# Kernel optimization log

Measured on AMD Instinct MI355X. Metric: run time of the kernel, lower is better.

Reference implementation:

```python
import jax, jax.numpy as jnp
import numpy as np

B, L, H = 2, 2048, 2048
NH, NKV, HD = 16, 8, 128
K = 4            # conv kernel size
BASE = 1000000.0 # rotary base
H2 = NH // 2
N_REP = NH // NKV


def setup_inputs() -> dict:
    key = jax.random.key(0)
    ks = jax.random.split(key, 12)
    s = 0.02
    hidden_states = jax.random.normal(ks[0], (B, L, H), jnp.float32)
    idx = jnp.arange(L)
    diff = (idx[:, None] - idx[None, :]).astype(jnp.float32)
    # lightning-attention decay mask: -(i-j) on/below diagonal, -1e9 above
    lin_attention_mask = jnp.where(diff >= 0, -diff, -1e9).astype(jnp.float32)
    # additive causal mask for softmax half
    attention_mask = jnp.where(diff >= 0, 0.0, -1e9).astype(jnp.float32)[None, None]
    # ALiBi-style positive per-head slopes for the linear half
    slope_rate = (2.0 ** (-8.0 * jnp.arange(1, H2 + 1, dtype=jnp.float32) / H2)).reshape(H2, 1, 1)
    position_ids = jnp.arange(L, dtype=jnp.int32)
    Wq = s * jax.random.normal(ks[1], (H, H), jnp.float32)
    bq = jnp.zeros((H,), jnp.float32)
    Wk = s * jax.random.normal(ks[2], (H, NKV * HD), jnp.float32)
    bk = jnp.zeros((NKV * HD,), jnp.float32)
    Wv = s * jax.random.normal(ks[3], (H, NKV * HD), jnp.float32)
    bv = jnp.zeros((NKV * HD,), jnp.float32)
    Wo = s * jax.random.normal(ks[4], (H, H), jnp.float32)
    # conv init: identity tap at last index + tiny noise (matches _init_conv_to_one)
    q_conv_w = jnp.zeros((H // 2, K), jnp.float32).at[:, K - 1].set(1.0) + 1e-4 * jax.random.normal(ks[5], (H // 2, K), jnp.float32)
    q_conv_b = jnp.zeros((H // 2,), jnp.float32)
    k_conv_w = jnp.zeros((NKV * HD, K), jnp.float32).at[:, K - 1].set(1.0) + 1e-4 * jax.random.normal(ks[6], (NKV * HD, K), jnp.float32)
    k_conv_b = jnp.zeros((NKV * HD,), jnp.float32)
    return dict(hidden_states=hidden_states, lin_attention_mask=lin_attention_mask,
                attention_mask=attention_mask, slope_rate=slope_rate, position_ids=position_ids,
                Wq=Wq, bq=bq, Wk=Wk, bk=bk, Wv=Wv, bv=bv, Wo=Wo,
                q_conv_w=q_conv_w, q_conv_b=q_conv_b, k_conv_w=k_conv_w, k_conv_b=k_conv_b)


def _dwconv_causal(x, w, b):
    # x: [B,L,C]; w: [C,K]; b: [C]. Causal depthwise conv (torch Conv1d cross-correlation,
    # padding K-1 then truncate to first L positions).
    xp = jnp.pad(x, ((0, 0), (K - 1, 0), (0, 0)))
    y = b
    for i in range(K):
        y = y + xp[:, i:i + x.shape[1], :] * w[:, i]
    return y


def _rot_half(x):
    return jnp.concatenate([-x[..., HD // 2:], x[..., :HD // 2]], axis=-1)


def _rep_kv(x):
    # [B,NKV,L,D] -> [B,NH,L,D] via repeat_interleave on head dim
    return jnp.repeat(x, N_REP, axis=1)


def reference(hidden_states, lin_attention_mask, attention_mask, slope_rate, position_ids,
              Wq, bq, Wk, bk, Wv, bv, Wo, q_conv_w, q_conv_b, k_conv_w, k_conv_b):
    q = hidden_states @ Wq + bq          # [B,L,H]
    k = hidden_states @ Wk + bk          # [B,L,NKV*HD]
    v = hidden_states @ Wv + bv          # [B,L,NKV*HD]

    # ---- softmax half (first NH//2 heads, rotary) ----
    qs = q[..., :H // 2].reshape(B, L, H2, HD).transpose(0, 2, 1, 3)   # [B,H2,L,D]
    ks_ = k.reshape(B, L, NKV, HD).transpose(0, 2, 1, 3)               # [B,NKV,L,D]
    vs = v.reshape(B, L, NKV, HD).transpose(0, 2, 1, 3)
    inv_freq = 1.0 / (BASE ** (jnp.arange(0, HD, 2, dtype=jnp.float32) / HD))
    freqs = position_ids.astype(jnp.float32)[:, None] * inv_freq[None, :]
    emb = jnp.concatenate([freqs, freqs], axis=-1)                     # [L,D]
    cos, sin = jnp.cos(emb)[None, None], jnp.sin(emb)[None, None]
    qs = qs * cos + _rot_half(qs) * sin
    kr = ks_ * cos + _rot_half(ks_) * sin
    k_soft = _rep_kv(kr)[:, :H2]
    v_soft = _rep_kv(vs)[:, :H2]
    attn = jnp.einsum('bhnd,bhmd->bhnm', qs, k_soft) / np.sqrt(HD).astype(np.float32)
    attn = attn + attention_mask
    attn = jax.nn.softmax(attn.astype(jnp.float32), axis=-1).astype(qs.dtype)
    attn_out = jnp.einsum('bhnm,bhmd->bhnd', attn, v_soft)
    attn_out = attn_out.transpose(0, 2, 1, 3).reshape(B, L, H // 2)

    # ---- linear half (last NH//2 heads: conv -> silu -> decayed linear attention) ----
    q_tnorm = _dwconv_causal(q[..., H // 2:], q_conv_w, q_conv_b)      # [B,L,H/2]
    kc = _dwconv_causal(k, k_conv_w, k_conv_b)                          # [B,L,NKV*HD]
    qt = jax.nn.silu(q_tnorm).reshape(B, L, H2, HD).transpose(0, 2, 1, 3)
    kc = jax.nn.silu(kc).reshape(B, L, NKV, HD).transpose(0, 2, 1, 3)
    k_lin = _rep_kv(kc)[:, H2:]
    v_lin = _rep_kv(vs)[:, H2:]
    lin_mask = jnp.exp(slope_rate * lin_attention_mask)                 # [H2,L,L]
    energy = jnp.einsum('bhnd,bhmd->bhnm', qt, k_lin) * lin_mask
    out_t = jnp.einsum('bhnm,bhmd->bhnd', energy, v_lin)
    out_t = out_t.transpose(0, 2, 1, 3).reshape(B, L, H // 2)
    # SimpleRMSNorm (no weight), computed in fp32
    ot32 = out_t.astype(jnp.float32)
    out_t = (ot32 * jax.lax.rsqrt(jnp.mean(ot32 * ot32, axis=-1, keepdims=True) + 1e-6)).astype(out_t.dtype)

    return jnp.concatenate([attn_out, out_t], axis=-1) @ Wo
```

## Files before the change

kernel.cpp:

```cpp
#include <hip/hip_runtime.h>
#include <hip/hip_bf16.h>

typedef __attribute__((ext_vector_type(8))) short short8;
typedef __attribute__((ext_vector_type(4))) float f32x4;
typedef __attribute__((ext_vector_type(16))) float f32x16;

__device__ __forceinline__ void gl_lds16(const void* g, void* l) {
    void* gp = const_cast<void*>(g);
    __builtin_amdgcn_global_load_lds((__attribute__((address_space(1))) void*)gp,
                                     (__attribute__((address_space(3))) void*)l, 16, 0, 0);
}
__device__ __forceinline__ short f2bf(float f) {
    __hip_bfloat16 h = __float2bfloat16(f);
    return __builtin_bit_cast(short, h);
}
__device__ __forceinline__ float bf2f(__hip_bfloat16 h) { return __bfloat162float(h); }
__device__ __forceinline__ float bfbits2f(short s) {
    unsigned int u = ((unsigned int)(unsigned short)s) << 16;
    return __builtin_bit_cast(float, u);
}
__device__ __forceinline__ void store_val(float* C, size_t i, float v) { C[i] = v; }
__device__ __forceinline__ void store_val(__hip_bfloat16* C, size_t i, float v) { C[i] = __float2bfloat16(v); }

__global__ __launch_bounds__(256) void pre_kernel(
    const float* __restrict__ hs, __hip_bfloat16* __restrict__ hsb,
    const float* __restrict__ bq, const float* __restrict__ bk, const float* __restrict__ bv,
    float* __restrict__ bqkv,
    const float* __restrict__ Wq, const float* __restrict__ Wo,
    const float* __restrict__ Wk, const float* __restrict__ Wv,
    __hip_bfloat16* __restrict__ oq, __hip_bfloat16* __restrict__ oo, __hip_bfloat16* __restrict__ okv)
{
    __shared__ float tile[64][65];
    int bx = blockIdx.x, t = threadIdx.x;
    if (bx < 8192) {
        size_t i = (size_t)bx * 256 + t;
        float4 v = ((const float4*)hs)[i];
        ushort4 o;
        o.x = (unsigned short)f2bf(v.x); o.y = (unsigned short)f2bf(v.y);
        o.z = (unsigned short)f2bf(v.z); o.w = (unsigned short)f2bf(v.w);
        ((ushort4*)hsb)[i] = o;
    } else if (bx < 8208) {
        int i = (bx - 8192) * 256 + t;
        bqkv[i] = (i < 2048) ? bq[i] : ((i < 3072) ? bk[i - 2048] : bv[i - 3072]);
    } else {
        int idx = bx - 8208;
        int z = idx >> 10, rem = idx & 1023;
        const float* in; __hip_bfloat16* out; int C;
        if (z == 0)      { in = Wq; out = oq; C = 2048; }
        else if (z == 1) { in = Wo; out = oo; C = 2048; }
        else if (z == 2) { in = Wk; out = okv; C = 1024; }
        else             { in = Wv; out = okv + (size_t)1024 * 2048; C = 1024; }
        int c0 = (rem & 31) * 64, r0 = (rem >> 5) * 64;
        if (c0 >= C) return;
        int tx = t & 15, ty = t >> 4;
#pragma unroll
        for (int i = 0; i < 4; ++i) {
            float4 v = *(const float4*)(in + (size_t)(r0 + ty + i * 16) * C + c0 + tx * 4);
            tile[ty + i * 16][tx * 4 + 0] = v.x; tile[ty + i * 16][tx * 4 + 1] = v.y;
            tile[ty + i * 16][tx * 4 + 2] = v.z; tile[ty + i * 16][tx * 4 + 3] = v.w;
        }
        __syncthreads();
#pragma unroll
        for (int i = 0; i < 4; ++i) {
            int lc = ty + i * 16, lr0 = tx * 4;
            ushort4 o;
            o.x = (unsigned short)f2bf(tile[lr0 + 0][lc]);
            o.y = (unsigned short)f2bf(tile[lr0 + 1][lc]);
            o.z = (unsigned short)f2bf(tile[lr0 + 2][lc]);
            o.w = (unsigned short)f2bf(tile[lr0 + 3][lc]);
            *(ushort4*)(out + (size_t)(c0 + lc) * 2048 + r0 + lr0) = o;
        }
    }
}

__global__ __launch_bounds__(256) void gemm_qkv_kernel(
    const __hip_bfloat16* __restrict__ A, const __hip_bfloat16* __restrict__ Bt,
    const float* __restrict__ bias, __hip_bfloat16* __restrict__ C, __hip_bfloat16* __restrict__ C2,
    int M, int N, int K)
{
    __shared__ short As[128 * 64];
    __shared__ short Bs[128 * 64];
    int t = threadIdx.x, lane = t & 63, w = t >> 6;
    int m0 = blockIdx.y * 128, n0 = blockIdx.x * 128;
    int wr = (w >> 1) * 64, wc = (w & 1) * 64;
    f32x16 acc[2][2];
#pragma unroll
    for (int i = 0; i < 2; ++i)
#pragma unroll
        for (int j = 0; j < 2; ++j)
#pragma unroll
            for (int e = 0; e < 16; ++e) acc[i][j][e] = 0.f;
    int srow = w * 8 + (lane >> 3);
    int scol = ((lane & 7) ^ (lane >> 3)) * 8;
    const __hip_bfloat16* Ag = A + (size_t)(m0 + srow) * K + scol;
    const __hip_bfloat16* Bg = Bt + (size_t)(n0 + srow) * K + scol;
    short* AsB = As + w * 8 * 64;
    short* BsB = Bs + w * 8 * 64;
    int l31 = lane & 31, khalf = lane >> 5;
    for (int k0 = 0; k0 < K; k0 += 64) {
#pragma unroll
        for (int it = 0; it < 4; ++it) {
            gl_lds16(Ag + (size_t)it * 32 * K + k0, AsB + it * 32 * 64);
            gl_lds16(Bg + (size_t)it * 32 * K + k0, BsB + it * 32 * 64);
        }
        __syncthreads();
#pragma unroll
        for (int s = 0; s < 4; ++s) {
            int chunk = s * 2 + khalf;
            short8 a[2], b[2];
#pragma unroll
            for (int mi = 0; mi < 2; ++mi) {
                int row = wr + mi * 32 + l31;
                a[mi] = *(const short8*)&As[row * 64 + ((chunk ^ (row & 7)) * 8)];
            }
#pragma unroll
            for (int ni = 0; ni < 2; ++ni) {
                int row = wc + ni * 32 + l31;
                b[ni] = *(const short8*)&Bs[row * 64 + ((chunk ^ (row & 7)) * 8)];
            }
#pragma unroll
            for (int mi = 0; mi < 2; ++mi)
#pragma unroll
                for (int ni = 0; ni < 2; ++ni)
                    acc[mi][ni] = __builtin_amdgcn_mfma_f32_32x32x16_bf16(a[mi], b[ni], acc[mi][ni], 0, 0, 0);
        }
        __syncthreads();
    }
    bool hi = (n0 + wc) >= 2048;
    __hip_bfloat16* Cw = hi ? C2 : C;
    int nbase = (n0 + wc) - (hi ? 2048 : 0);
#pragma unroll
    for (int ni = 0; ni < 2; ++ni) {
        float bias_v = bias[n0 + wc + ni * 32 + l31];
        int n = nbase + ni * 32 + l31;
#pragma unroll
        for (int mi = 0; mi < 2; ++mi) {
#pragma unroll
            for (int reg = 0; reg < 16; ++reg) {
                int m = m0 + wr + mi * 32 + (reg & 3) + 8 * (reg >> 2) + 4 * khalf;
                Cw[(size_t)m * 2048 + n] = __float2bfloat16(acc[mi][ni][reg] + bias_v);
            }
        }
    }
}

__global__ __launch_bounds__(256) void gemm_out_kernel(
    const __hip_bfloat16* __restrict__ A, const __hip_bfloat16* __restrict__ Bt,
    float* __restrict__ C, int M, int N, int K)
{
    __shared__ short As[64 * 64];
    __shared__ short Bs[128 * 64];
    int t = threadIdx.x, lane = t & 63, w = t >> 6;
    int m0 = blockIdx.y * 64, n0 = blockIdx.x * 128;
    f32x16 acc[2];
#pragma unroll
    for (int i = 0; i < 2; ++i)
#pragma unroll
        for (int e = 0; e < 16; ++e) acc[i][e] = 0.f;
    int srow = w * 8 + (lane >> 3);
    int scol = ((lane & 7) ^ (lane >> 3)) * 8;
    const __hip_bfloat16* Ag = A + (size_t)(m0 + srow) * K + scol;
    const __hip_bfloat16* Bg = Bt + (size_t)(n0 + srow) * K + scol;
    short* AsB = As + w * 8 * 64;
    short* BsB = Bs + w * 8 * 64;
    int l31 = lane & 31, khalf = lane >> 5;
    for (int k0 = 0; k0 < K; k0 += 64) {
#pragma unroll
        for (int it = 0; it < 2; ++it)
            gl_lds16(Ag + (size_t)it * 32 * K + k0, AsB + it * 32 * 64);
#pragma unroll
        for (int it = 0; it < 4; ++it)
            gl_lds16(Bg + (size_t)it * 32 * K + k0, BsB + it * 32 * 64);
        __syncthreads();
#pragma unroll
        for (int s = 0; s < 4; ++s) {
            int chunk = s * 2 + khalf;
            short8 a[2], b;
#pragma unroll
            for (int mi = 0; mi < 2; ++mi) {
                int row = mi * 32 + l31;
                a[mi] = *(const short8*)&As[row * 64 + ((chunk ^ (row & 7)) * 8)];
            }
            {
                int row = w * 32 + l31;
                b = *(const short8*)&Bs[row * 64 + ((chunk ^ (row & 7)) * 8)];
            }
#pragma unroll
            for (int mi = 0; mi < 2; ++mi)
                acc[mi] = __builtin_amdgcn_mfma_f32_32x32x16_bf16(a[mi], b, acc[mi], 0, 0, 0);
        }
        __syncthreads();
    }
    int n = n0 + w * 32 + l31;
#pragma unroll
    for (int mi = 0; mi < 2; ++mi) {
#pragma unroll
        for (int reg = 0; reg < 16; ++reg) {
            int m = m0 + mi * 32 + (reg & 3) + 8 * (reg >> 2) + 4 * khalf;
            C[(size_t)m * N + n] = acc[mi][reg];
        }
    }
}

__global__ __launch_bounds__(256) void prep_kernel(
    const __hip_bfloat16* __restrict__ qf, const __hip_bfloat16* __restrict__ kvf,
    const int* __restrict__ pid,
    const float* __restrict__ qw, const float* __restrict__ qb,
    const float* __restrict__ kw, const float* __restrict__ kb,
    __hip_bfloat16* __restrict__ Qs, __hip_bfloat16* __restrict__ qt,
    __hip_bfloat16* __restrict__ Ks, __hip_bfloat16* __restrict__ kc,
    __hip_bfloat16* __restrict__ Vt)
{
    __shared__ __hip_bfloat16 tile[32][33];
    int bx = blockIdx.x, t = threadIdx.x;
    if (bx < 32768) {
        size_t idx = (size_t)bx * 256 + t;
        int c = idx & 2047; int l = (int)((idx >> 11) & 2047); int b = (int)(idx >> 22);
        size_t row = (size_t)(b * 2048 + l) * 2048;
        if (c < 1024) {
            int h = c >> 7, d = c & 127, j = d & 63;
            float posv = (float)pid[l];
            float ang = posv * expf(-0.21586735246819178f * (float)j);
            float cs = cosf(ang), sn = sinf(ang);
            float x = bf2f(qf[row + c]);
            float xr = (d < 64) ? -bf2f(qf[row + c + 64]) : bf2f(qf[row + c - 64]);
            Qs[(((size_t)(b * 8 + h) * 2048) + l) * 128 + d] = __float2bfloat16(x * cs + xr * sn);
        } else {
            int ch = c - 1024;
            float y = qb[ch];
#pragma unroll
            for (int i = 0; i < 4; ++i) {
                int ls = l - 3 + i;
                if (ls >= 0) y += qw[ch * 4 + i] * bf2f(qf[(size_t)(b * 2048 + ls) * 2048 + 1024 + ch]);
            }
            y = y / (1.f + __expf(-y));
            qt[(((size_t)(b * 8 + (ch >> 7)) * 2048) + l) * 128 + (ch & 127)] = __float2bfloat16(y);
        }
    } else if (bx < 49152) {
        size_t idx = (size_t)(bx - 32768) * 256 + t;
        int cc = idx & 1023; int l = (int)((idx >> 10) & 2047); int b = (int)(idx >> 21);
        size_t row = (size_t)(b * 2048 + l) * 2048;
        if (cc < 512) {
            int kvh = cc >> 7, d = cc & 127, j = d & 63;
            float posv = (float)pid[l];
            float ang = posv * expf(-0.21586735246819178f * (float)j);
            float cs = cosf(ang), sn = sinf(ang);
            float x = bf2f(kvf[row + cc]);
            float xr = (d < 64) ? -bf2f(kvf[row + cc + 64]) : bf2f(kvf[row + cc - 64]);
            Ks[(((size_t)(b * 4 + kvh) * 2048) + l) * 128 + d] = __float2bfloat16(x * cs + xr * sn);
        } else {
            float y = kb[cc];
#pragma unroll
            for (int i = 0; i < 4; ++i) {
                int ls = l - 3 + i;
                if (ls >= 0) y += kw[cc * 4 + i] * bf2f(kvf[(size_t)(b * 2048 + ls) * 2048 + cc]);
            }
            y = y / (1.f + __expf(-y));
            kc[(((size_t)(b * 4 + ((cc - 512) >> 7)) * 2048) + l) * 128 + (cc & 127)] = __float2bfloat16(y);
        }
    } else {
        int idx = bx - 49152;
        int bh = idx >> 8, rem = idx & 255;
        int d0 = (rem >> 6) * 32, l0 = (rem & 63) * 32;
        int b = bh >> 3, kvh = bh & 7;
        int tx = t & 31, ty = t >> 5;
#pragma unroll
        for (int i = 0; i < 4; ++i)
            tile[ty + i*8][tx] = kvf[(size_t)(b * 2048 + l0 + ty + i*8) * 2048 + 1024 + kvh * 128 + d0 + tx];
        __syncthreads();
#pragma unroll
        for (int i = 0; i < 4; ++i)
            Vt[(size_t)(bh * 128 + d0 + ty + i*8) * 2048 + l0 + tx] = tile[tx][ty + i*8];
    }
}

__device__ __forceinline__ float redsum16(float v) {
    v += __shfl_xor(v, 1); v += __shfl_xor(v, 2);
    v += __shfl_xor(v, 4); v += __shfl_xor(v, 8);
    return v;
}
__device__ __forceinline__ void decode_slice(int x, int& q, int& jl, int& jh) {
    int sub;
    if (x < 8)       { q = x; sub = 0; }
    else if (x < 24) { q = 8 + ((x - 8) >> 1); sub = (x - 8) & 1; }
    else if (x < 48) { int u = x - 24; int d = u / 3; q = 16 + d; sub = u - 3 * d; }
    else             { int u = x - 48; q = 24 + (u >> 2); sub = u & 3; }
    jl = sub * 8;
    jh = min(jl + 8, q + 1);
}
__device__ __forceinline__ int slice_base(int q) {
    if (q < 8)  return q;
    if (q < 16) return 8 + 2 * (q - 8);
    if (q < 24) return 24 + 3 * (q - 16);
    return 48 + 4 * (q - 24);
}

__global__ __launch_bounds__(256, 4) void attn_part_kernel(
    const __hip_bfloat16* __restrict__ Qs, const __hip_bfloat16* __restrict__ Ks,
    const __hip_bfloat16* __restrict__ Vt,
    const __hip_bfloat16* __restrict__ Qb, const __hip_bfloat16* __restrict__ Kb,
    const float* __restrict__ slope,
    __hip_bfloat16* __restrict__ partOf, float* __restrict__ partL,
    __hip_bfloat16* __restrict__ partOl)
{
    __shared__ short Kt[64 * 128];
    __shared__ short Vl[128 * 64];
    __shared__ short Pl[4][16 * 64];
    int bxr = blockIdx.x, bh = blockIdx.y;
    int x = bxr >> 1;
    bool is_lin = (bxr & 1);
    int q, jl, jh; decode_slice(x, q, jl, jh);
    int b = bh >> 3, h = bh & 7;
    int t = threadIdx.x, lane = t & 63, w = t >> 6, quad = lane >> 4, c0 = lane & 15;
    int rk = t >> 4, ck = (t & 15) ^ rk;
    int rv = t >> 3, cv = (t & 7) ^ (rv & 7);
    int gi0 = q * 64 + w * 16;
    float s = 0.f;
    if (is_lin) {
        s = slope[h];
        float thr = ((float)(q * 64) - 63.f - 25.f / s) * (1.f / 64.f);
        int jlo = thr > 0.f ? (int)ceilf(thr) : 0;
        if (jlo > q) jlo = q;
        if (jlo > jl) jl = jlo;
        if (jl >= jh) return;
    }
    const __hip_bfloat16* Qbase = is_lin ? Qb : Qs;
    const __hip_bfloat16* Kbase = is_lin ? Kb : Ks;
    const __hip_bfloat16* Qrow = Qbase + ((size_t)(b * 8 + h) * 2048 + q * 64 + w * 16 + c0) * 128;
    short8 qa[4];
#pragma unroll
    for (int kk = 0; kk < 4; ++kk) qa[kk] = *(const short8*)(Qrow + kk * 32 + quad * 8);
    const char* Kg = (const char*)(Kbase + ((size_t)(b * 4 + (h >> 1)) * 2048) * 128);
    const __hip_bfloat16* Vg = Vt + (size_t)(b * 8 + (is_lin ? 4 : 0) + (h >> 1)) * 128 * 2048;
    f32x4 O[8];
#pragma unroll
    for (int v = 0; v < 8; ++v) O[v] = (f32x4){0.f, 0.f, 0.f, 0.f};
    float lacc[4] = {0.f, 0.f, 0.f, 0.f};
    const float scale = 0.08838834764831845f;
    for (int j0 = jl; j0 < jh; ++j0) {
#pragma unroll
        for (int it = 0; it < 4; ++it) {
            gl_lds16(Kg + (size_t)(j0 * 64 + it * 16 + rk) * 256 + ck * 16, (char*)Kt + it * 4096 + w * 1024);
            gl_lds16((const char*)(Vg + (size_t)(it * 32 + rv) * 2048 + j0 * 64 + cv * 8), (char*)Vl + it * 4096 + w * 1024);
        }
        __syncthreads();
        f32x4 S[4];
#pragma unroll
        for (int ni = 0; ni < 4; ++ni) S[ni] = (f32x4){0.f, 0.f, 0.f, 0.f};
#pragma unroll
        for (int kk = 0; kk < 4; ++kk) {
#pragma unroll
            for (int ni = 0; ni < 4; ++ni) {
                short8 bb = *(const short8*)&Kt[(ni * 16 + c0) * 128 + (((kk * 4 + quad) ^ c0) * 8)];
                S[ni] = __builtin_amdgcn_mfma_f32_16x16x32_bf16(qa[kk], bb, S[ni], 0, 0, 0);
            }
        }
        bool diag = (j0 == q);
        if (!is_lin) {
#pragma unroll
            for (int ni = 0; ni < 4; ++ni) {
                int gj = j0 * 64 + ni * 16 + c0;
#pragma unroll
                for (int r = 0; r < 4; ++r) {
                    int gi = gi0 + quad * 4 + r;
                    float p = (diag && gj > gi) ? 0.f : __expf(S[ni][r] * scale);
                    lacc[r] += p;
                    int m = quad * 4 + r;
                    Pl[w][m * 64 + (((ni * 2 + (c0 >> 3)) ^ (m & 7)) * 8) + (c0 & 7)] = f2bf(p);
                }
            }
        } else {
#pragma unroll
            for (int ni = 0; ni < 4; ++ni) {
                int gj = j0 * 64 + ni * 16 + c0;
#pragma unroll
                for (int r = 0; r < 4; ++r) {
                    int gi = gi0 + quad * 4 + r;
                    float p = 0.f;
                    if (!diag || gj <= gi) p = S[ni][r] * __expf(s * (float)(gj - gi));
                    int m = quad * 4 + r;
                    Pl[w][m * 64 + (((ni * 2 + (c0 >> 3)) ^ (m & 7)) * 8) + (c0 & 7)] = f2bf(p);
                }
            }
        }
#pragma unroll
        for (int kk = 0; kk < 2; ++kk) {
            short8 a = *(const short8*)&Pl[w][c0 * 64 + (((kk * 4 + quad) ^ (c0 & 7)) * 8)];
#pragma unroll
            for (int v = 0; v < 8; ++v) {
                short8 bb = *(const short8*)&Vl[(v * 16 + c0) * 64 + (((kk * 4 + quad) ^ (c0 & 7)) * 8)];
                O[v] = __builtin_amdgcn_mfma_f32_16x16x32_bf16(a, bb, O[v], 0, 0, 0);
            }
        }
        __syncthreads();
    }
    if (!is_lin) {
#pragma unroll
        for (int r = 0; r < 4; ++r) {
            float lr = redsum16(lacc[r]);
            if (c0 == 0) partL[((size_t)(bh * 80 + x)) * 64 + w * 16 + quad * 4 + r] = lr;
        }
    }
    __hip_bfloat16* po = (is_lin ? partOl : partOf) + (size_t)(bh * 80 + x) * 64 * 128;
#pragma unroll
    for (int v = 0; v < 8; ++v)
#pragma unroll
        for (int r = 0; r < 4; ++r)
            po[(size_t)(w * 16 + quad * 4 + r) * 128 + v * 16 + c0] = __float2bfloat16(O[v][r]);
}

__global__ __launch_bounds__(256) void merge_kernel(
    const __hip_bfloat16* __restrict__ partOf, const float* __restrict__ partL,
    const __hip_bfloat16* __restrict__ partOl, const float* __restrict__ slope,
    __hip_bfloat16* __restrict__ CC)
{
    int bx = blockIdx.x, t = threadIdx.x;
    if (bx < 512) {
        int q = bx & 31, bh = bx >> 5, b = bh >> 3, h = bh & 7;
        int row = t >> 2, cg = (t & 3) * 32;
        int base = slice_base(q), ns = (q + 8) >> 3;
        float lt = 0.f;
        float acc[32];
#pragma unroll
        for (int i = 0; i < 32; ++i) acc[i] = 0.f;
        for (int s = 0; s < ns; ++s) {
            size_t sb = (size_t)(bh * 80 + base + s);
            lt += partL[sb * 64 + row];
            const short* po = (const short*)partOf + (sb * 64 + row) * 128 + cg;
#pragma unroll
            for (int g = 0; g < 4; ++g) {
                short8 vv = *(const short8*)(po + g * 8);
#pragma unroll
                for (int e = 0; e < 8; ++e) acc[g * 8 + e] += bfbits2f(vv[e]);
            }
        }
        float inv = 1.f / lt;
        __hip_bfloat16* co = CC + ((size_t)(b * 2048 + q * 64 + row)) * 2048 + h * 128 + cg;
#pragma unroll
        for (int g = 0; g < 4; ++g) {
            short8 o;
#pragma unroll
            for (int e = 0; e < 8; ++e) o[e] = f2bf(acc[g * 8 + e] * inv);
            *(short8*)(co + g * 8) = o;
        }
    } else {
        int idx = bx - 512;
        int q = idx & 31, rg = (idx >> 5) & 3, b = idx >> 7;
        int row = rg * 16 + (t >> 4);
        int seg = t & 15;
        int hh = seg >> 1;
        int cs = (seg & 1) * 64;
        int bh = b * 8 + hh;
        int base = slice_base(q), ns = (q + 8) >> 3;
        float s = slope[hh];
        float thr = ((float)(q * 64) - 63.f - 25.f / s) * (1.f / 64.f);
        int jlo = thr > 0.f ? (int)ceilf(thr) : 0;
        if (jlo > q) jlo = q;
        float acc[64];
#pragma unroll
        for (int i = 0; i < 64; ++i) acc[i] = 0.f;
        for (int s_ = 0; s_ < ns; ++s_) {
            int jl2 = s_ * 8, jh2 = min(jl2 + 8, q + 1);
            if (max(jl2, jlo) >= jh2) continue;
            const short* po = (const short*)partOl + ((size_t)(bh * 80 + base + s_) * 64 + row) * 128 + cs;
#pragma unroll
            for (int g = 0; g < 8; ++g) {
                short8 vv = *(const short8*)(po + g * 8);
#pragma unroll
                for (int e = 0; e < 8; ++e) acc[g * 8 + e] += bfbits2f(vv[e]);
            }
        }
        float ss = 0.f;
#pragma unroll
        for (int i = 0; i < 64; ++i) ss += acc[i] * acc[i];
        ss = redsum16(ss);
        float rs = rsqrtf(ss * (1.f / 1024.f) + 1e-6f);
        __hip_bfloat16* co = CC + ((size_t)(b * 2048 + q * 64 + row)) * 2048 + 1024 + hh * 128 + cs;
#pragma unroll
        for (int g = 0; g < 8; ++g) {
            short8 o;
#pragma unroll
            for (int e = 0; e < 8; ++e) o[e] = f2bf(acc[g * 8 + e] * rs);
            *(short8*)(co + g * 8) = o;
        }
    }
}

extern "C" void kernel_launch(void* const* d_in, const int* in_sizes, int n_in,
                              void* d_out, int out_size, void* d_ws, size_t ws_size,
                              hipStream_t stream) {
    const float* hs   = (const float*)d_in[0];
    const float* slope= (const float*)d_in[3];
    const int*   pid  = (const int*)d_in[4];
    const float* Wq   = (const float*)d_in[5];
    const float* bq   = (const float*)d_in[6];
    const float* Wk   = (const float*)d_in[7];
    const float* bk   = (const float*)d_in[8];
    const float* Wv   = (const float*)d_in[9];
    const float* bv   = (const float*)d_in[10];
    const float* Wo   = (const float*)d_in[11];
    const float* qcw  = (const float*)d_in[12];
    const float* qcb  = (const float*)d_in[13];
    const float* kcw  = (const float*)d_in[14];
    const float* kcb  = (const float*)d_in[15];
    float* out = (float*)d_out;

    char* p = (char*)d_ws;
    auto alloc = [&](size_t bytes) { char* r = p; p += (bytes + 255) & ~(size_t)255; return r; };
    __hip_bfloat16* hsb   = (__hip_bfloat16*)alloc((size_t)4096 * 2048 * 2);
    __hip_bfloat16* bWqT  = (__hip_bfloat16*)alloc((size_t)2048 * 2048 * 2);
    __hip_bfloat16* bWkvT = (__hip_bfloat16*)alloc((size_t)2048 * 2048 * 2);
    __hip_bfloat16* bWoT  = (__hip_bfloat16*)alloc((size_t)2048 * 2048 * 2);
    float*          bqkv  = (float*)alloc(4096 * 4);
    __hip_bfloat16* qf    = (__hip_bfloat16*)alloc((size_t)4096 * 2048 * 2);
    __hip_bfloat16* kvf   = (__hip_bfloat16*)alloc((size_t)4096 * 2048 * 2);
    __hip_bfloat16* Qsb   = (__hip_bfloat16*)alloc((size_t)2 * 8 * 2048 * 128 * 2);
    __hip_bfloat16* Ksb   = (__hip_bfloat16*)alloc((size_t)2 * 4 * 2048 * 128 * 2);
    __hip_bfloat16* Vtb   = (__hip_bfloat16*)alloc((size_t)2 * 8 * 128 * 2048 * 2);
    __hip_bfloat16* qtb   = (__hip_bfloat16*)alloc((size_t)2 * 8 * 2048 * 128 * 2);
    __hip_bfloat16* kcbuf = (__hip_bfloat16*)alloc((size_t)2 * 4 * 2048 * 128 * 2);
    __hip_bfloat16* CC    = (__hip_bfloat16*)alloc((size_t)4096 * 2048 * 2);

    __hip_bfloat16* partOf = (__hip_bfloat16*)hsb;
    __hip_bfloat16* partOl = (__hip_bfloat16*)qf;
    float*          partL  = (float*)((char*)kvf + (size_t)8 * 1024 * 1024);

    pre_kernel<<<12304, 256, 0, stream>>>(hs, hsb, bq, bk, bv, bqkv, Wq, Wo, Wk, Wv, bWqT, bWoT, bWkvT);

    gemm_qkv_kernel<<<dim3(32, 32), 256, 0, stream>>>(hsb, bWqT, bqkv, qf, kvf, 4096, 4096, 2048);

    prep_kernel<<<53248, 256, 0, stream>>>(qf, kvf, pid, qcw, qcb, kcw, kcb, Qsb, qtb, Ksb, kcbuf, Vtb);

    attn_part_kernel<<<dim3(160, 16), 256, 0, stream>>>(Qsb, Ksb, Vtb, qtb, kcbuf, slope, partOf, partL, partOl);
    merge_kernel<<<768, 256, 0, stream>>>(partOf, partL, partOl, slope, CC);

    gemm_out_kernel<<<dim3(16, 64), 256, 0, stream>>>(CC, bWoT, out, 4096, 2048, 2048);
}
```

Baseline: 429.3 us.

## Unify GEMMs into double-buffered 16x16x32 MFMA kernel with BK=32

Replaces the two single-buffered GEMM kernels with one templated kernel that double-buffers LDS tiles with K-step 32. The next tile's global-to-LDS load is issued before computing the current one, with one barrier per iteration. It switches from 32x32x16 to 16x16x32 MFMA with a 4x4 accumulator grid per wave. The output GEMM moves from 64x128 to 128x128 tiles, which halves its grid. The halved grid may reduce occupancy, and the smaller K step means more iterations and barriers.

Result: slower. 440.5 us (+2.6%).

```diff
diff --git a/kernel.cpp b/kernel.cpp
--- a/kernel.cpp
+++ b/kernel.cpp
@@ -3,7 +3,6 @@
 
 typedef __attribute__((ext_vector_type(8))) short short8;
 typedef __attribute__((ext_vector_type(4))) float f32x4;
-typedef __attribute__((ext_vector_type(16))) float f32x16;
 
 __device__ __forceinline__ void gl_lds16(const void* g, void* l) {
     void* gp = const_cast<void*>(g);
@@ -73,131 +72,74 @@
     }
 }
 
-__global__ __launch_bounds__(256) void gemm_qkv_kernel(
+template <typename OutT, bool HAS_BIAS, bool SPLIT>
+__global__ __launch_bounds__(256) void gemm_db_kernel(
     const __hip_bfloat16* __restrict__ A, const __hip_bfloat16* __restrict__ Bt,
-    const float* __restrict__ bias, __hip_bfloat16* __restrict__ C, __hip_bfloat16* __restrict__ C2,
+    const float* __restrict__ bias, OutT* __restrict__ C, OutT* __restrict__ C2,
     int M, int N, int K)
 {
-    __shared__ short As[128 * 64];
-    __shared__ short Bs[128 * 64];
+    __shared__ short As[2][128 * 32];
+    __shared__ short Bs[2][128 * 32];
     int t = threadIdx.x, lane = t & 63, w = t >> 6;
     int m0 = blockIdx.y * 128, n0 = blockIdx.x * 128;
     int wr = (w >> 1) * 64, wc = (w & 1) * 64;
-    f32x16 acc[2][2];
-#pragma unroll
-    for (int i = 0; i < 2; ++i)
-#pragma unroll
-        for (int j = 0; j < 2; ++j)
-#pragma unroll
-            for (int e = 0; e < 16; ++e) acc[i][j][e] = 0.f;
-    int srow = w * 8 + (lane >> 3);
-    int scol = ((lane & 7) ^ (lane >> 3)) * 8;
-    const __hip_bfloat16* Ag = A + (size_t)(m0 + srow) * K + scol;
-    const __hip_bfloat16* Bg = Bt + (size_t)(n0 + srow) * K + scol;
-    short* AsB = As + w * 8 * 64;
-    short* BsB = Bs + w * 8 * 64;
-    int l31 = lane & 31, khalf = lane >> 5;
-    for (int k0 = 0; k0 < K; k0 += 64) {
-#pragma unroll
-        for (int it = 0; it < 4; ++it) {
-            gl_lds16(Ag + (size_t)it * 32 * K + k0, AsB + it * 32 * 64);
-            gl_lds16(Bg + (size_t)it * 32 * K + k0, BsB + it * 32 * 64);
-        }
+    int quad = lane >> 4, c0 = lane & 15;
+    f32x4 acc[4][4];
+#pragma unroll
+    for (int i = 0; i < 4; ++i)
+#pragma unroll
+        for (int j = 0; j < 4; ++j) acc[i][j] = (f32x4){0.f, 0.f, 0.f, 0.f};
+    int srow0 = w * 16 + (lane >> 2);
+    int srow1 = (4 + w) * 16 + (lane >> 2);
+    int sc = ((lane & 3) ^ ((lane >> 3) & 3)) * 8;
+    const __hip_bfloat16* Ag0 = A + (size_t)(m0 + srow0) * K + sc;
+    const __hip_bfloat16* Ag1 = A + (size_t)(m0 + srow1) * K + sc;
+    const __hip_bfloat16* Bg0 = Bt + (size_t)(n0 + srow0) * K + sc;
+    const __hip_bfloat16* Bg1 = Bt + (size_t)(n0 + srow1) * K + sc;
+    int rs = (quad ^ ((c0 >> 1) & 3)) * 8;
+    gl_lds16(Ag0, &As[0][w * 512]);
+    gl_lds16(Ag1, &As[0][(4 + w) * 512]);
+    gl_lds16(Bg0, &Bs[0][w * 512]);
+    gl_lds16(Bg1, &Bs[0][(4 + w) * 512]);
+    int niter = K >> 5;
+    for (int kt = 0; kt < niter; ++kt) {
+        int cur = kt & 1;
         __syncthreads();
-#pragma unroll
-        for (int s = 0; s < 4; ++s) {
-            int chunk = s * 2 + khalf;
-            short8 a[2], b[2];
-#pragma unroll
-            for (int mi = 0; mi < 2; ++mi) {
-                int row = wr + mi * 32 + l31;
-                a[mi] = *(const short8*)&As[row * 64 + ((chunk ^ (row & 7)) * 8)];
-            }
-#pragma unroll
-            for (int ni = 0; ni < 2; ++ni) {
-                int row = wc + ni * 32 + l31;
-                b[ni] = *(const short8*)&Bs[row * 64 + ((chunk ^ (row & 7)) * 8)];
-            }
-#pragma unroll
-            for (int mi = 0; mi < 2; ++mi)
-#pragma unroll
-                for (int ni = 0; ni < 2; ++ni)
-                    acc[mi][ni] = __builtin_amdgcn_mfma_f32_32x32x16_bf16(a[mi], b[ni], acc[mi][ni], 0, 0, 0);
-        }
-        __syncthreads();
-    }
-    bool hi = (n0 + wc) >= 2048;
-    __hip_bfloat16* Cw = hi ? C2 : C;
-    int nbase = (n0 + wc) - (hi ? 2048 : 0);
-#pragma unroll
-    for (int ni = 0; ni < 2; ++ni) {
-        float bias_v = bias[n0 + wc + ni * 32 + l31];
-        int n = nbase + ni * 32 + l31;
-#pragma unroll
-        for (int mi = 0; mi < 2; ++mi) {
-#pragma unroll
-            for (int reg = 0; reg < 16; ++reg) {
-                int m = m0 + wr + mi * 32 + (reg & 3) + 8 * (reg >> 2) + 4 * khalf;
-                Cw[(size_t)m * 2048 + n] = __float2bfloat16(acc[mi][ni][reg] + bias_v);
-            }
-        }
-    }
-}
-
-__global__ __launch_bounds__(256) void gemm_out_kernel(
-    const __hip_bfloat16* __restrict__ A, const __hip_bfloat16* __restrict__ Bt,
-    float* __restrict__ C, int M, int N, int K)
-{
-    __shared__ short As[64 * 64];
-    __shared__ short Bs[128 * 64];
-    int t = threadIdx.x, lane = t & 63, w = t >> 6;
-    int m0 = blockIdx.y * 64, n0 = blockIdx.x * 128;
-    f32x16 acc[2];
-#pragma unroll
-    for (int i = 0; i < 2; ++i)
-#pragma unroll
-        for (int e = 0; e < 16; ++e) acc[i][e] = 0.f;
-    int srow = w * 8 + (lane >> 3);
-    int scol = ((lane & 7) ^ (lane >> 3)) * 8;
-    const __hip_bfloat16* Ag = A + (size_t)(m0 + srow) * K + scol;
-    const __hip_bfloat16* Bg = Bt + (size_t)(n0 + srow) * K + scol;
-    short* AsB = As + w * 8 * 64;
-    short* BsB = Bs + w * 8 * 64;
-    int l31 = lane & 31, khalf = lane >> 5;
-    for (int k0 = 0; k0 < K; k0 += 64) {
-#pragma unroll
-        for (int it = 0; it < 2; ++it)
-            gl_lds16(Ag + (size_t)it * 32 * K + k0, AsB + it * 32 * 64);
-#pragma unroll
-        for (int it = 0; it < 4; ++it)
-            gl_lds16(Bg + (size_t)it * 32 * K + k0, BsB + it * 32 * 64);
-        __syncthreads();
-#pragma unroll
-        for (int s = 0; s < 4; ++s) {
-            int chunk = s * 2 + khalf;
-            short8 a[2], b;
-#pragma unroll
-            for (int mi = 0; mi < 2; ++mi) {
-                int row = mi * 32 + l31;
-                a[mi] = *(const short8*)&As[row * 64 + ((chunk ^ (row & 7)) * 8)];
-            }
-            {
-                int row = w * 32 + l31;
-                b = *(const short8*)&Bs[row * 64 + ((chunk ^ (row & 7)) * 8)];
-            }
-#pragma unroll
-            for (int mi = 0; mi < 2; ++mi)
-                acc[mi] = __builtin_amdgcn_mfma_f32_32x32x16_bf16(a[mi], b, acc[mi], 0, 0, 0);
-        }
-        __syncthreads();
-    }
-    int n = n0 + w * 32 + l31;
-#pragma unroll
-    for (int mi = 0; mi < 2; ++mi) {
-#pragma unroll
-        for (int reg = 0; reg < 16; ++reg) {
-            int m = m0 + mi * 32 + (reg & 3) + 8 * (reg >> 2) + 4 * khalf;
-            C[(size_t)m * N + n] = acc[mi][reg];
+        if (kt + 1 < niter) {
+            int k0n = (kt + 1) << 5;
+            gl_lds16(Ag0 + k0n, &As[1 - cur][w * 512]);
+            gl_lds16(Ag1 + k0n, &As[1 - cur][(4 + w) * 512]);
+            gl_lds16(Bg0 + k0n, &Bs[1 - cur][w * 512]);
+            gl_lds16(Bg1 + k0n, &Bs[1 - cur][(4 + w) * 512]);
+        }
+        short8 a[4], b[4];
+#pragma unroll
+        for (int mi = 0; mi < 4; ++mi)
+            a[mi] = *(const short8*)&As[cur][(wr + mi * 16 + c0) * 32 + rs];
+#pragma unroll
+        for (int ni = 0; ni < 4; ++ni)
+            b[ni] = *(const short8*)&Bs[cur][(wc + ni * 16 + c0) * 32 + rs];
+#pragma unroll
+        for (int mi = 0; mi < 4; ++mi)
+#pragma unroll
+            for (int ni = 0; ni < 4; ++ni)
+                acc[mi][ni] = __builtin_amdgcn_mfma_f32_16x16x32_bf16(a[mi], b[ni], acc[mi][ni], 0, 0, 0);
+    }
+    bool hi = SPLIT && (n0 + wc) >= 2048;
+    OutT* Cw = hi ? C2 : C;
+    int nbase = SPLIT ? ((n0 + wc) - (hi ? 2048 : 0)) : (n0 + wc);
+    int Nw = SPLIT ? 2048 : N;
+#pragma unroll
+    for (int ni = 0; ni < 4; ++ni) {
+        int n = nbase + ni * 16 + c0;
+        float bias_v = HAS_BIAS ? bias[n0 + wc + ni * 16 + c0] : 0.f;
+#pragma unroll
+        for (int mi = 0; mi < 4; ++mi) {
+#pragma unroll
+            for (int r = 0; r < 4; ++r) {
+                int m = m0 + wr + mi * 16 + quad * 4 + r;
+                store_val(Cw, (size_t)m * Nw + n, acc[mi][ni][r] + bias_v);
+            }
         }
     }
 }
@@ -527,12 +469,14 @@
 
     pre_kernel<<<12304, 256, 0, stream>>>(hs, hsb, bq, bk, bv, bqkv, Wq, Wo, Wk, Wv, bWqT, bWoT, bWkvT);
 
-    gemm_qkv_kernel<<<dim3(32, 32), 256, 0, stream>>>(hsb, bWqT, bqkv, qf, kvf, 4096, 4096, 2048);
+    gemm_db_kernel<__hip_bfloat16, true, true><<<dim3(32, 32), 256, 0, stream>>>(
+        hsb, bWqT, bqkv, qf, kvf, 4096, 4096, 2048);
 
     prep_kernel<<<53248, 256, 0, stream>>>(qf, kvf, pid, qcw, qcb, kcw, kcb, Qsb, qtb, Ksb, kcbuf, Vtb);
 
     attn_part_kernel<<<dim3(160, 16), 256, 0, stream>>>(Qsb, Ksb, Vtb, qtb, kcbuf, slope, partOf, partL, partOl);
     merge_kernel<<<768, 256, 0, stream>>>(partOf, partL, partOl, slope, CC);
 
-    gemm_out_kernel<<<dim3(16, 64), 256, 0, stream>>>(CC, bWoT, out, 4096, 2048, 2048);
-}
+    gemm_db_kernel<float, false, false><<<dim3(16, 32), 256, 0, stream>>>(
+        CC, bWoT, nullptr, out, nullptr, 4096, 2048, 2048);
+}
```
